# Optimization experiments

Hardware: AMD Instinct MI355X
Metric: run time of the kernel (lower is better)

The kernel has to match this reference:

```python
import jax, jax.numpy as jnp
import numpy as np

EMBED = 192
HEADS = 6
WIN = (7, 7, 7)
B = 256
NW = 64  # number of distinct window masks; b // NW = true batch
N = WIN[0] * WIN[1] * WIN[2]  # 343 tokens per window


def _rel_pos_index(win):
    # Faithful port of the torch buffer construction.
    coords = np.stack(np.meshgrid(np.arange(win[0]), np.arange(win[1]), np.arange(win[2]), indexing='ij'))
    cf = coords.reshape(3, -1)                     # [3, N]
    rel = cf[:, :, None] - cf[:, None, :]          # [3, N, N]
    rel = rel.transpose(1, 2, 0).copy()            # [N, N, 3]
    rel[..., 0] += win[0] - 1
    rel[..., 1] += win[1] - 1
    rel[..., 2] += win[2] - 1
    rel[..., 0] *= (2 * win[1] - 1) * (2 * win[2] - 1)
    rel[..., 1] *= (2 * win[2] - 1)
    return rel.sum(-1).astype(np.int32)            # [N, N]


def setup_inputs() -> dict:
    key = jax.random.key(0)
    ks = jax.random.split(key, 8)
    table_size = (2 * WIN[0] - 1) * (2 * WIN[1] - 1) * (2 * WIN[2] - 1)  # 2197
    return {
        'x_in': jax.random.normal(ks[0], (B, N, EMBED), dtype=jnp.float32),
        'x_cross': jax.random.normal(ks[1], (B, N, EMBED), dtype=jnp.float32),
        'mask': jnp.zeros((NW, N, N), dtype=jnp.float32),
        'q_w': jax.random.normal(ks[2], (EMBED, EMBED), dtype=jnp.float32) * 0.02,
        'kv_w': jax.random.normal(ks[3], (2 * EMBED, EMBED), dtype=jnp.float32) * 0.02,
        'proj_w': jax.random.normal(ks[4], (EMBED, EMBED), dtype=jnp.float32) * 0.02,
        'proj_b': jnp.zeros((EMBED,), dtype=jnp.float32),
        'bias_table': jax.random.normal(ks[5], (table_size, HEADS), dtype=jnp.float32) * 0.02,
        'rel_idx': jnp.asarray(_rel_pos_index(WIN)),
    }


def reference(x_in, x_cross, mask, q_w, kv_w, proj_w, proj_b, bias_table, rel_idx):
    b, n, c = x_in.shape
    h = HEADS
    hd = c // h
    scale = hd ** -0.5
    # Projections (torch Linear: y = x @ W^T), no qkv bias
    q = (x_in @ q_w.T).reshape(b, n, h, hd).transpose(0, 2, 1, 3) * scale   # [b,h,n,hd]
    kv = (x_cross @ kv_w.T).reshape(b, n, 2, h, hd)
    k = kv[:, :, 0].transpose(0, 2, 1, 3)                                   # [b,h,n,hd]
    v = kv[:, :, 1].transpose(0, 2, 1, 3)                                   # [b,h,n,hd]
    attn = jnp.einsum('bhqd,bhkd->bhqk', q, k)                              # [b,h,n,n]
    # Gathered relative position bias
    bias = bias_table[rel_idx[:n, :n].reshape(-1)].reshape(n, n, h).transpose(2, 0, 1)
    attn = attn + bias[None]
    # Window mask add: [b//nw, nw, h, n, n] + [1, nw, 1, n, n]
    nw = mask.shape[0]
    attn = attn.reshape(b // nw, nw, h, n, n) + mask[None, :, None]
    attn = attn.reshape(b, h, n, n)
    attn = jax.nn.softmax(attn, axis=-1)
    x = jnp.einsum('bhqk,bhkd->bhqd', attn, v).transpose(0, 2, 1, 3).reshape(b, n, c)
    return x @ proj_w.T + proj_b
```

## Files before the change

kernel.cpp:

```cpp
#include <hip/hip_runtime.h>

#define NTOK 343
#define NPAD 352
#define CEMB 192
#define NH   6
#define HD   32
#define NB   256
#define NWIN 64

typedef __attribute__((ext_vector_type(8))) short short8;
typedef __attribute__((ext_vector_type(4))) float f32x4;
typedef __attribute__((ext_vector_type(4))) unsigned int uint4v;
typedef __attribute__((ext_vector_type(2))) unsigned int uint2v;

__device__ __forceinline__ unsigned short f2bf(float f) {
    unsigned int u = __builtin_bit_cast(unsigned int, f);
    u += 0x7fffu + ((u >> 16) & 1u);
    return (unsigned short)(u >> 16);
}
__device__ __forceinline__ float bf2f(unsigned short h) {
    unsigned int u = ((unsigned int)h) << 16;
    return __builtin_bit_cast(float, u);
}
__device__ __forceinline__ short8 pack8(float4 f0, float4 f1) {
    short8 r;
    r[0] = (short)f2bf(f0.x); r[1] = (short)f2bf(f0.y);
    r[2] = (short)f2bf(f0.z); r[3] = (short)f2bf(f0.w);
    r[4] = (short)f2bf(f1.x); r[5] = (short)f2bf(f1.y);
    r[6] = (short)f2bf(f1.z); r[7] = (short)f2bf(f1.w);
    return r;
}
__device__ __forceinline__ unsigned int cvt_pk_bf16(float lo, float hi) {
    unsigned int r;
    asm("v_cvt_pk_bf16_f32 %0, %1, %2" : "=v"(r) : "v"(lo), "v"(hi));
    return r;
}

#define LOG2E 1.4426950408889634f

__global__ void prep_weights(const float* __restrict__ qw, const float* __restrict__ kvw,
                             const float* __restrict__ pw,
                             unsigned short* __restrict__ qwb, unsigned short* __restrict__ kvwb,
                             unsigned short* __restrict__ pwb) {
    const float scale = 0.17677669529663689f * LOG2E;
    int idx = blockIdx.x * 256 + threadIdx.x;
    if (idx < 36864)        qwb[idx] = f2bf(qw[idx] * scale);
    else if (idx < 110592)  kvwb[idx - 36864] = f2bf(kvw[idx - 36864]);
    else if (idx < 147456)  pwb[idx - 110592] = f2bf(pw[idx - 110592]);
}

__global__ void prep_biasN(const float* __restrict__ table, const int* __restrict__ rel,
                           unsigned short* __restrict__ biasN) {
    __shared__ int sidx[32 * 33];
    int bid = blockIdx.x;
    int qt = bid / 11, kt = bid - qt * 11;
    int q0 = qt * 32, k0 = kt * 32;
    for (int e = threadIdx.x; e < 1024; e += 256) {
        int i = e >> 5, j = e & 31;
        int q = q0 + i, k = k0 + j;
        sidx[i * 33 + j] = (q < NTOK && k < NTOK) ? rel[q * NTOK + k] : -1;
    }
    __syncthreads();
    for (int h = 0; h < NH; h++) {
        for (int e = threadIdx.x; e < 1024; e += 256) {
            int qq = e >> 5, kk = e & 31;
            int idx = sidx[qq * 33 + kk];
            float v = (idx >= 0) ? table[idx * NH + h] * LOG2E : 0.f;
            biasN[((size_t)h * NPAD + (q0 + qq)) * NPAD + (k0 + kk)] = f2bf(v);
        }
    }
}

__global__ void prep_maskN(const float* __restrict__ mask, unsigned short* __restrict__ maskN) {
    int idx = blockIdx.x * 256 + threadIdx.x;
    int w = idx / (NPAD * NPAD);
    int rem = idx - w * (NPAD * NPAD);
    int q = rem / NPAD, k = rem - q * NPAD;
    float v = (q < NTOK && k < NTOK) ? mask[((size_t)w * NTOK + q) * NTOK + k] * LOG2E : 0.f;
    maskN[idx] = f2bf(v);
}

__global__ __launch_bounds__(512, 2)
void qkv_kernel(const float* __restrict__ x_in, const float* __restrict__ x_cross,
                const unsigned short* __restrict__ qwb, const unsigned short* __restrict__ kvwb,
                unsigned short* __restrict__ Qb, unsigned short* __restrict__ Kb,
                unsigned short* __restrict__ Vtb) {
    extern __shared__ char smem[];
    unsigned short* Ws = (unsigned short*)smem;
    const int tid = threadIdx.x;
    const int wave = tid >> 6, lane = tid & 63;
    const int quad = lane >> 4, l16 = lane & 15;
    const int b = blockIdx.x / 3, o = blockIdx.x % 3;
    const float* xsrc = (o == 0) ? x_in : x_cross;
    const unsigned short* wsrc = (o == 0) ? qwb : (o == 1 ? kvwb : (kvwb + 192 * CEMB));
    const f32x4 zero4 = {0.f, 0.f, 0.f, 0.f};

    for (int i = tid; i < 4608; i += 512) {
        int r = i / 24, c8 = i - r * 24;
        *(short8*)(Ws + r * 200 + c8 * 8) = *(const short8*)(wsrc + (size_t)r * CEMB + c8 * 8);
    }
    __syncthreads();

    for (int mi = 0; mi < 3; mi++) {
        int mt = wave + (mi << 3);
        if (mt >= 22) continue;
        int row = mt * 16 + l16;
        f32x4 acc[12];
#pragma unroll
        for (int nt = 0; nt < 12; nt++) acc[nt] = zero4;
#pragma unroll
        for (int kc = 0; kc < 6; kc++) {
            short8 a = {};
            if (row < NTOK) {
                const float* xp = xsrc + ((size_t)b * NTOK + row) * CEMB + kc * 32 + (quad << 3);
                float4 f0 = *(const float4*)xp;
                float4 f1 = *(const float4*)(xp + 4);
                a = pack8(f0, f1);
            }
#pragma unroll
            for (int nt = 0; nt < 12; nt++) {
                const short8 bf = *(const short8*)(Ws + (nt * 16 + l16) * 200 + kc * 32 + (quad << 3));
                acc[nt] = __builtin_amdgcn_mfma_f32_16x16x32_bf16(a, bf, acc[nt], 0, 0, 0);
            }
        }
        if (o < 2) {
            unsigned short* dst = (o == 0 ? Qb : Kb) + (size_t)b * NPAD * CEMB;
#pragma unroll
            for (int nt = 0; nt < 12; nt++) {
#pragma unroll
                for (int r = 0; r < 4; r++) {
                    int m = mt * 16 + (quad << 2) + r;
                    dst[(size_t)m * CEMB + nt * 16 + l16] = f2bf(acc[nt][r]);
                }
            }
        } else {
#pragma unroll
            for (int nt = 0; nt < 12; nt++) {
                int h = nt >> 1, d = ((nt & 1) << 4) + l16;
#pragma unroll
                for (int r = 0; r < 4; r++) {
                    int m = mt * 16 + (quad << 2) + r;
                    Vtb[(((size_t)b * NH + h) * 32 + d) * 360 + m] = f2bf(acc[nt][r]);
                }
            }
        }
    }
}

__global__ __launch_bounds__(512, 6)
void attn_kernel(const unsigned short* __restrict__ Qb, const unsigned short* __restrict__ Kb,
                 const unsigned short* __restrict__ Vtb,
                 const unsigned short* __restrict__ biasN, const unsigned short* __restrict__ maskN,
                 unsigned short* __restrict__ attnb) {
    extern __shared__ char smem[];
    unsigned short* Ks = (unsigned short*)smem;
    unsigned short* Vt = (unsigned short*)(smem + 28160);

    const int tid = threadIdx.x;
    const int wave = tid >> 6, lane = tid & 63;
    const int quad = lane >> 4, l16 = lane & 15;
    const int q4 = quad << 2, q8 = quad << 3;
    const int p = blockIdx.x;
    const int L = (p & 7) * 192 + (p >> 3);
    const int w = L / 24, r_ = L - w * 24;
    const int b = (r_ / 6) * 64 + w;
    const int h = r_ - (r_ / 6) * 6;
    const f32x4 zero4 = {0.f, 0.f, 0.f, 0.f};

    for (int i = tid; i < 1408; i += 512) {
        int key = i >> 2, part = i & 3;
        *(short8*)(Ks + key * 40 + part * 8) =
            *(const short8*)(Kb + ((size_t)b * NPAD + key) * CEMB + h * 32 + part * 8);
    }
    const unsigned short* vsrc = Vtb + (size_t)(b * NH + h) * 32 * 360;
    for (int i = tid; i < 1440; i += 512) {
        *(short8*)(Vt + i * 8) = *(const short8*)(vsrc + i * 8);
    }
    short8 qa[3] = {};
#pragma unroll
    for (int i = 0; i < 3; i++) {
        int mt = wave + (i << 3);
        if (mt < 22)
            qa[i] = *(const short8*)(Qb + ((size_t)b * NPAD + mt * 16 + l16) * CEMB + h * 32 + q8);
    }
    __syncthreads();

    const unsigned short* biasNp = biasN + (size_t)h * NPAD * NPAD;
    const unsigned short* maskNp = maskN + (size_t)w * NPAD * NPAD;
#pragma unroll
    for (int i = 0; i < 3; i++) {
        int mt = wave + (i << 3);
        if (mt >= 22) continue;
        const int q = mt * 16 + l16;
        const unsigned short* brow = biasNp + (size_t)q * NPAD;
        const unsigned short* mrow = maskNp + (size_t)q * NPAD;
        float rp = 0.f;
        f32x4 o0 = zero4, o1 = zero4;
        ushort4 bt0c = *(const ushort4*)(brow + q4);
        ushort4 mk0c = *(const ushort4*)(mrow + q4);
        ushort4 bt1c = *(const ushort4*)(brow + 16 + q4);
        ushort4 mk1c = *(const ushort4*)(mrow + 16 + q4);
        for (int ch = 0; ch < 11; ch++) {
            const int kb_ = ch * 32;
            const int kbn = (ch < 10) ? kb_ + 32 : kb_;
            ushort4 bt0n = *(const ushort4*)(brow + kbn + q4);
            ushort4 mk0n = *(const ushort4*)(mrow + kbn + q4);
            ushort4 bt1n = *(const ushort4*)(brow + kbn + 16 + q4);
            ushort4 mk1n = *(const ushort4*)(mrow + kbn + 16 + q4);
            const short8 k0f = *(const short8*)(Ks + (kb_ + l16) * 40 + q8);
            const short8 k1f = *(const short8*)(Ks + (kb_ + 16 + l16) * 40 + q8);
            f32x4 s0 = __builtin_amdgcn_mfma_f32_16x16x32_bf16(k0f, qa[i], zero4, 0, 0, 0);
            f32x4 s1 = __builtin_amdgcn_mfma_f32_16x16x32_bf16(k1f, qa[i], zero4, 0, 0, 0);
            float p00 = __builtin_amdgcn_exp2f(s0[0] + bf2f(bt0c.x) + bf2f(mk0c.x));
            float p01 = __builtin_amdgcn_exp2f(s0[1] + bf2f(bt0c.y) + bf2f(mk0c.y));
            float p02 = __builtin_amdgcn_exp2f(s0[2] + bf2f(bt0c.z) + bf2f(mk0c.z));
            float p03 = __builtin_amdgcn_exp2f(s0[3] + bf2f(bt0c.w) + bf2f(mk0c.w));
            float p10 = __builtin_amdgcn_exp2f(s1[0] + bf2f(bt1c.x) + bf2f(mk1c.x));
            float p11 = __builtin_amdgcn_exp2f(s1[1] + bf2f(bt1c.y) + bf2f(mk1c.y));
            float p12 = __builtin_amdgcn_exp2f(s1[2] + bf2f(bt1c.z) + bf2f(mk1c.z));
            float p13 = __builtin_amdgcn_exp2f(s1[3] + bf2f(bt1c.w) + bf2f(mk1c.w));
            if (ch == 10) {
                if (q4 + 0 >= 7) p10 = 0.f;
                if (q4 + 1 >= 7) p11 = 0.f;
                if (q4 + 2 >= 7) p12 = 0.f;
                if (q4 + 3 >= 7) p13 = 0.f;
            }
            rp += ((p00 + p01) + (p02 + p03)) + ((p10 + p11) + (p12 + p13));
            unsigned int c0 = cvt_pk_bf16(p00, p01);
            unsigned int c1 = cvt_pk_bf16(p02, p03);
            unsigned int c2 = cvt_pk_bf16(p10, p11);
            unsigned int c3 = cvt_pk_bf16(p12, p13);
            uint2v sa = __builtin_amdgcn_permlane32_swap(c0, c2, false, false);
            uint2v sb = __builtin_amdgcn_permlane32_swap(c1, c3, false, false);
            uint2v ta = __builtin_amdgcn_permlane16_swap(sa[0], sa[1], false, false);
            uint2v tb = __builtin_amdgcn_permlane16_swap(sb[0], sb[1], false, false);
            const short8 pa = __builtin_bit_cast(short8, (uint4v){ta[0], tb[0], ta[1], tb[1]});
            const short8 v0 = *(const short8*)(Vt + l16 * 360 + kb_ + q8);
            const short8 v1 = *(const short8*)(Vt + (16 + l16) * 360 + kb_ + q8);
            o0 = __builtin_amdgcn_mfma_f32_16x16x32_bf16(pa, v0, o0, 0, 0, 0);
            o1 = __builtin_amdgcn_mfma_f32_16x16x32_bf16(pa, v1, o1, 0, 0, 0);
            bt0c = bt0n; mk0c = mk0n; bt1c = bt1n; mk1c = mk1n;
        }
        rp += __shfl_xor(rp, 16);
        rp += __shfl_xor(rp, 32);
        float inv = 1.f / rp;
#pragma unroll
        for (int r = 0; r < 4; r++) {
            float invr = __shfl(inv, (lane & 48) | (q4 + r));
            int n = mt * 16 + q4 + r;
            if (n < NTOK) {
                size_t base = ((size_t)b * NTOK + n) * CEMB + h * 32;
                attnb[base + l16] = f2bf(o0[r] * invr);
                attnb[base + 16 + l16] = f2bf(o1[r] * invr);
            }
        }
    }
}

__global__ __launch_bounds__(512, 2)
void proj_kernel(const unsigned short* __restrict__ attnb, const unsigned short* __restrict__ pwb,
                 const float* __restrict__ proj_b, float* __restrict__ out) {
    extern __shared__ char smem[];
    unsigned short* Ws = (unsigned short*)smem;
    const int tid = threadIdx.x;
    const int wave = tid >> 6, lane = tid & 63;
    const int quad = lane >> 4, l16 = lane & 15;
    for (int i = tid; i < 4608; i += 512) {
        int r = i / 24, c8 = i - r * 24;
        *(short8*)(Ws + r * 200 + c8 * 8) = *(const short8*)(pwb + (size_t)r * CEMB + c8 * 8);
    }
    float pb[12];
#pragma unroll
    for (int nt = 0; nt < 12; nt++) pb[nt] = proj_b[nt * 16 + l16];
    __syncthreads();

    const int mt = blockIdx.x * 8 + wave;
    const f32x4 zero4 = {0.f, 0.f, 0.f, 0.f};
    f32x4 acc[12];
#pragma unroll
    for (int nt = 0; nt < 12; nt++) acc[nt] = zero4;
#pragma unroll
    for (int ks = 0; ks < 6; ks++) {
        const short8 a = *(const short8*)(attnb + ((size_t)mt * 16 + l16) * CEMB + ks * 32 + (quad << 3));
#pragma unroll
        for (int nt = 0; nt < 12; nt++) {
            const short8 bfrag = *(const short8*)(Ws + (nt * 16 + l16) * 200 + ks * 32 + (quad << 3));
            acc[nt] = __builtin_amdgcn_mfma_f32_16x16x32_bf16(a, bfrag, acc[nt], 0, 0, 0);
        }
    }
#pragma unroll
    for (int nt = 0; nt < 12; nt++) {
#pragma unroll
        for (int r = 0; r < 4; r++) {
            int m = mt * 16 + (quad << 2) + r;
            out[(size_t)m * CEMB + nt * 16 + l16] = acc[nt][r] + pb[nt];
        }
    }
}

extern "C" void kernel_launch(void* const* d_in, const int* in_sizes, int n_in,
                              void* d_out, int out_size, void* d_ws, size_t ws_size,
                              hipStream_t stream) {
    (void)in_sizes; (void)n_in; (void)out_size; (void)ws_size;
    const float* x_in    = (const float*)d_in[0];
    const float* x_cross = (const float*)d_in[1];
    const float* mask    = (const float*)d_in[2];
    const float* q_w     = (const float*)d_in[3];
    const float* kv_w    = (const float*)d_in[4];
    const float* proj_w  = (const float*)d_in[5];
    const float* proj_b  = (const float*)d_in[6];
    const float* btab    = (const float*)d_in[7];
    const int*   rel     = (const int*)d_in[8];
    float* out = (float*)d_out;
    char* ws = (char*)d_ws;

    unsigned short* qwb   = (unsigned short*)(ws + 0);
    unsigned short* kvwb  = (unsigned short*)(ws + 73728);
    unsigned short* pwb   = (unsigned short*)(ws + 221184);
    unsigned short* biasN = (unsigned short*)(ws + 294912);
    unsigned short* maskN = (unsigned short*)(ws + 1781760);
    unsigned short* attnb = (unsigned short*)(ws + 17641472);
    unsigned short* Qb    = (unsigned short*)(ws + 51359744);
    unsigned short* Kb    = (unsigned short*)(ws + 85962752);
    unsigned short* Vtb   = (unsigned short*)(ws + 120565760);

    prep_weights<<<576, 256, 0, stream>>>(q_w, kv_w, proj_w, qwb, kvwb, pwb);
    prep_biasN<<<121, 256, 0, stream>>>(btab, rel, biasN);
    prep_maskN<<<30976, 256, 0, stream>>>(mask, maskN);
    qkv_kernel<<<NB * 3, 512, 76800, stream>>>(x_in, x_cross, qwb, kvwb, Qb, Kb, Vtb);
    attn_kernel<<<NB * NH, 512, 51200, stream>>>(Qb, Kb, Vtb, biasN, maskN, attnb);
    proj_kernel<<<686, 512, 76800, stream>>>(attnb, pwb, proj_b, out);
}
```

Measured before the change: 411.5 us.

## Store bias and mask in MFMA fragment order and fold into accumulator init

```diff
diff --git a/kernel.cpp b/kernel.cpp
--- a/kernel.cpp
+++ b/kernel.cpp
@@ -7,6 +7,7 @@
 #define HD   32
 #define NB   256
 #define NWIN 64
+#define FPLANE 123904
 
 typedef __attribute__((ext_vector_type(8))) short short8;
 typedef __attribute__((ext_vector_type(4))) float f32x4;
@@ -49,55 +50,62 @@
     else if (idx < 147456)  pwb[idx - 110592] = f2bf(pw[idx - 110592]);
 }
 
-__global__ void prep_biasN(const float* __restrict__ table, const int* __restrict__ rel,
-                           unsigned short* __restrict__ biasN) {
-    __shared__ int sidx[32 * 33];
-    int bid = blockIdx.x;
-    int qt = bid / 11, kt = bid - qt * 11;
-    int q0 = qt * 32, k0 = kt * 32;
-    for (int e = threadIdx.x; e < 1024; e += 256) {
-        int i = e >> 5, j = e & 31;
-        int q = q0 + i, k = k0 + j;
-        sidx[i * 33 + j] = (q < NTOK && k < NTOK) ? rel[q * NTOK + k] : -1;
-    }
-    __syncthreads();
-    for (int h = 0; h < NH; h++) {
-        for (int e = threadIdx.x; e < 1024; e += 256) {
-            int qq = e >> 5, kk = e & 31;
-            int idx = sidx[qq * 33 + kk];
-            float v = (idx >= 0) ? table[idx * NH + h] * LOG2E : 0.f;
-            biasN[((size_t)h * NPAD + (q0 + qq)) * NPAD + (k0 + kk)] = f2bf(v);
-        }
-    }
-}
-
-__global__ void prep_maskN(const float* __restrict__ mask, unsigned short* __restrict__ maskN) {
+__global__ void prep_biasF(const float* __restrict__ table, const int* __restrict__ rel,
+                           unsigned short* __restrict__ biasF) {
     int idx = blockIdx.x * 256 + threadIdx.x;
-    int w = idx / (NPAD * NPAD);
-    int rem = idx - w * (NPAD * NPAD);
-    int q = rem / NPAD, k = rem - q * NPAD;
-    float v = (q < NTOK && k < NTOK) ? mask[((size_t)w * NTOK + q) * NTOK + k] * LOG2E : 0.f;
-    maskN[idx] = f2bf(v);
+    int lane = idx & 63;
+    int rest = idx >> 6;
+    int t = rest & 1; rest >>= 1;
+    int ch = rest % 11; rest /= 11;
+    int mt = rest % 22; int h = rest / 22;
+    int q = mt * 16 + (lane & 15);
+    int k0 = ch * 32 + t * 16 + ((lane >> 4) << 2);
+    ushort4 out;
+#pragma unroll
+    for (int r = 0; r < 4; r++) {
+        int k = k0 + r;
+        float v = (q < NTOK && k < NTOK) ? table[rel[q * NTOK + k] * NH + h] * LOG2E : 0.f;
+        ((unsigned short*)&out)[r] = f2bf(v);
+    }
+    *(ushort4*)(biasF + (size_t)idx * 4) = out;
+}
+
+__global__ void prep_maskF(const float* __restrict__ mask, unsigned short* __restrict__ maskF) {
+    int idx = blockIdx.x * 256 + threadIdx.x;
+    int lane = idx & 63;
+    int rest = idx >> 6;
+    int t = rest & 1; rest >>= 1;
+    int ch = rest % 11; rest /= 11;
+    int mt = rest % 22; int w = rest / 22;
+    int q = mt * 16 + (lane & 15);
+    int k0 = ch * 32 + t * 16 + ((lane >> 4) << 2);
+    ushort4 out;
+#pragma unroll
+    for (int r = 0; r < 4; r++) {
+        int k = k0 + r;
+        float v;
+        if (k >= NTOK) v = -60000.f;
+        else if (q < NTOK) v = mask[((size_t)w * NTOK + q) * NTOK + k] * LOG2E;
+        else v = 0.f;
+        ((unsigned short*)&out)[r] = f2bf(v);
+    }
+    *(ushort4*)(maskF + (size_t)idx * 4) = out;
 }
 
 __global__ __launch_bounds__(512, 2)
-void qkv_kernel(const float* __restrict__ x_in, const float* __restrict__ x_cross,
-                const unsigned short* __restrict__ qwb, const unsigned short* __restrict__ kvwb,
-                unsigned short* __restrict__ Qb, unsigned short* __restrict__ Kb,
-                unsigned short* __restrict__ Vtb) {
+void qkv_q_kernel(const float* __restrict__ x_in, const unsigned short* __restrict__ qwb,
+                  unsigned short* __restrict__ Qb) {
     extern __shared__ char smem[];
     unsigned short* Ws = (unsigned short*)smem;
     const int tid = threadIdx.x;
     const int wave = tid >> 6, lane = tid & 63;
     const int quad = lane >> 4, l16 = lane & 15;
-    const int b = blockIdx.x / 3, o = blockIdx.x % 3;
-    const float* xsrc = (o == 0) ? x_in : x_cross;
-    const unsigned short* wsrc = (o == 0) ? qwb : (o == 1 ? kvwb : (kvwb + 192 * CEMB));
+    const int b = blockIdx.x;
     const f32x4 zero4 = {0.f, 0.f, 0.f, 0.f};
 
     for (int i = tid; i < 4608; i += 512) {
         int r = i / 24, c8 = i - r * 24;
-        *(short8*)(Ws + r * 200 + c8 * 8) = *(const short8*)(wsrc + (size_t)r * CEMB + c8 * 8);
+        *(short8*)(Ws + r * 200 + c8 * 8) = *(const short8*)(qwb + (size_t)r * CEMB + c8 * 8);
     }
     __syncthreads();
 
@@ -112,10 +120,8 @@
         for (int kc = 0; kc < 6; kc++) {
             short8 a = {};
             if (row < NTOK) {
-                const float* xp = xsrc + ((size_t)b * NTOK + row) * CEMB + kc * 32 + (quad << 3);
-                float4 f0 = *(const float4*)xp;
-                float4 f1 = *(const float4*)(xp + 4);
-                a = pack8(f0, f1);
+                const float* xp = x_in + ((size_t)b * NTOK + row) * CEMB + kc * 32 + (quad << 3);
+                a = pack8(*(const float4*)xp, *(const float4*)(xp + 4));
             }
 #pragma unroll
             for (int nt = 0; nt < 12; nt++) {
@@ -123,25 +129,104 @@
                 acc[nt] = __builtin_amdgcn_mfma_f32_16x16x32_bf16(a, bf, acc[nt], 0, 0, 0);
             }
         }
-        if (o < 2) {
-            unsigned short* dst = (o == 0 ? Qb : Kb) + (size_t)b * NPAD * CEMB;
+        unsigned short* dst = Qb + (size_t)b * NPAD * CEMB;
+#pragma unroll
+        for (int nt = 0; nt < 12; nt++) {
+#pragma unroll
+            for (int r = 0; r < 4; r++) {
+                int m = mt * 16 + (quad << 2) + r;
+                dst[(size_t)m * CEMB + nt * 16 + l16] = f2bf(acc[nt][r]);
+            }
+        }
+    }
+}
+
+__global__ __launch_bounds__(512, 2)
+void qkv_kv_kernel(const float* __restrict__ x_cross, const unsigned short* __restrict__ kvwb,
+                   unsigned short* __restrict__ Kb, unsigned short* __restrict__ Vtb) {
+    extern __shared__ char smem[];
+    unsigned short* Ws = (unsigned short*)smem;
+    const int tid = threadIdx.x;
+    const int wave = tid >> 6, lane = tid & 63;
+    const int quad = lane >> 4, l16 = lane & 15;
+    const int b = blockIdx.x;
+    const f32x4 zero4 = {0.f, 0.f, 0.f, 0.f};
+
+    for (int i = tid; i < 4608; i += 512) {
+        int r = i / 24, c8 = i - r * 24;
+        *(short8*)(Ws + r * 200 + c8 * 8) = *(const short8*)(kvwb + (size_t)r * CEMB + c8 * 8);
+    }
+
+    short8 a[3][6];
+#pragma unroll
+    for (int mi = 0; mi < 3; mi++) {
+        int mt = wave + (mi << 3);
+        int row = mt * 16 + l16;
+#pragma unroll
+        for (int kc = 0; kc < 6; kc++) {
+            a[mi][kc] = (short8){};
+            if (mt < 22 && row < NTOK) {
+                const float* xp = x_cross + ((size_t)b * NTOK + row) * CEMB + kc * 32 + (quad << 3);
+                a[mi][kc] = pack8(*(const float4*)xp, *(const float4*)(xp + 4));
+            }
+        }
+    }
+    __syncthreads();
+
+#pragma unroll
+    for (int mi = 0; mi < 3; mi++) {
+        int mt = wave + (mi << 3);
+        if (mt >= 22) continue;
+        f32x4 acc[12];
+#pragma unroll
+        for (int nt = 0; nt < 12; nt++) acc[nt] = zero4;
+#pragma unroll
+        for (int kc = 0; kc < 6; kc++) {
 #pragma unroll
             for (int nt = 0; nt < 12; nt++) {
-#pragma unroll
-                for (int r = 0; r < 4; r++) {
-                    int m = mt * 16 + (quad << 2) + r;
-                    dst[(size_t)m * CEMB + nt * 16 + l16] = f2bf(acc[nt][r]);
-                }
-            }
-        } else {
+                const short8 bf = *(const short8*)(Ws + (nt * 16 + l16) * 200 + kc * 32 + (quad << 3));
+                acc[nt] = __builtin_amdgcn_mfma_f32_16x16x32_bf16(a[mi][kc], bf, acc[nt], 0, 0, 0);
+            }
+        }
+        unsigned short* dst = Kb + (size_t)b * NPAD * CEMB;
+#pragma unroll
+        for (int nt = 0; nt < 12; nt++) {
+#pragma unroll
+            for (int r = 0; r < 4; r++) {
+                int m = mt * 16 + (quad << 2) + r;
+                dst[(size_t)m * CEMB + nt * 16 + l16] = f2bf(acc[nt][r]);
+            }
+        }
+    }
+    __syncthreads();
+    for (int i = tid; i < 4608; i += 512) {
+        int r = i / 24, c8 = i - r * 24;
+        *(short8*)(Ws + r * 200 + c8 * 8) = *(const short8*)(kvwb + (size_t)(192 + r) * CEMB + c8 * 8);
+    }
+    __syncthreads();
+
+#pragma unroll
+    for (int mi = 0; mi < 3; mi++) {
+        int mt = wave + (mi << 3);
+        if (mt >= 22) continue;
+        f32x4 acc[12];
+#pragma unroll
+        for (int nt = 0; nt < 12; nt++) acc[nt] = zero4;
+#pragma unroll
+        for (int kc = 0; kc < 6; kc++) {
 #pragma unroll
             for (int nt = 0; nt < 12; nt++) {
-                int h = nt >> 1, d = ((nt & 1) << 4) + l16;
-#pragma unroll
-                for (int r = 0; r < 4; r++) {
-                    int m = mt * 16 + (quad << 2) + r;
-                    Vtb[(((size_t)b * NH + h) * 32 + d) * 360 + m] = f2bf(acc[nt][r]);
-                }
+                const short8 bf = *(const short8*)(Ws + (nt * 16 + l16) * 200 + kc * 32 + (quad << 3));
+                acc[nt] = __builtin_amdgcn_mfma_f32_16x16x32_bf16(a[mi][kc], bf, acc[nt], 0, 0, 0);
+            }
+        }
+#pragma unroll
+        for (int nt = 0; nt < 12; nt++) {
+            int h = nt >> 1, d = ((nt & 1) << 4) + l16;
+#pragma unroll
+            for (int r = 0; r < 4; r++) {
+                int m = mt * 16 + (quad << 2) + r;
+                Vtb[(((size_t)b * NH + h) * 32 + d) * 360 + m] = f2bf(acc[nt][r]);
             }
         }
     }
@@ -150,7 +235,7 @@
 __global__ __launch_bounds__(512, 6)
 void attn_kernel(const unsigned short* __restrict__ Qb, const unsigned short* __restrict__ Kb,
                  const unsigned short* __restrict__ Vtb,
-                 const unsigned short* __restrict__ biasN, const unsigned short* __restrict__ maskN,
+                 const unsigned short* __restrict__ biasF, const unsigned short* __restrict__ maskF,
                  unsigned short* __restrict__ attnb) {
     extern __shared__ char smem[];
     unsigned short* Ks = (unsigned short*)smem;
@@ -185,53 +270,55 @@
     }
     __syncthreads();
 
-    const unsigned short* biasNp = biasN + (size_t)h * NPAD * NPAD;
-    const unsigned short* maskNp = maskN + (size_t)w * NPAD * NPAD;
+    const unsigned short* bF = biasF + (size_t)h * FPLANE;
+    const unsigned short* mF = maskF + (size_t)w * FPLANE;
+    const int lane4 = lane << 2;
 #pragma unroll
     for (int i = 0; i < 3; i++) {
         int mt = wave + (i << 3);
         if (mt >= 22) continue;
-        const int q = mt * 16 + l16;
-        const unsigned short* brow = biasNp + (size_t)q * NPAD;
-        const unsigned short* mrow = maskNp + (size_t)q * NPAD;
         float rp = 0.f;
         f32x4 o0 = zero4, o1 = zero4;
-        ushort4 bt0c = *(const ushort4*)(brow + q4);
-        ushort4 mk0c = *(const ushort4*)(mrow + q4);
-        ushort4 bt1c = *(const ushort4*)(brow + 16 + q4);
-        ushort4 mk1c = *(const ushort4*)(mrow + 16 + q4);
+        int off = mt * 5632;
+        ushort4 bt0c = *(const ushort4*)(bF + off + lane4);
+        ushort4 mk0c = *(const ushort4*)(mF + off + lane4);
+        ushort4 bt1c = *(const ushort4*)(bF + off + 256 + lane4);
+        ushort4 mk1c = *(const ushort4*)(mF + off + 256 + lane4);
         for (int ch = 0; ch < 11; ch++) {
             const int kb_ = ch * 32;
-            const int kbn = (ch < 10) ? kb_ + 32 : kb_;
-            ushort4 bt0n = *(const ushort4*)(brow + kbn + q4);
-            ushort4 mk0n = *(const ushort4*)(mrow + kbn + q4);
-            ushort4 bt1n = *(const ushort4*)(brow + kbn + 16 + q4);
-            ushort4 mk1n = *(const ushort4*)(mrow + kbn + 16 + q4);
+            const int offn = (ch < 10) ? off + 512 : off;
+            ushort4 bt0n = *(const ushort4*)(bF + offn + lane4);
+            ushort4 mk0n = *(const ushort4*)(mF + offn + lane4);
+            ushort4 bt1n = *(const ushort4*)(bF + offn + 256 + lane4);
+            ushort4 mk1n = *(const ushort4*)(mF + offn + 256 + lane4);
+            f32x4 c0, c1;
+            c0[0] = bf2f(bt0c.x) + bf2f(mk0c.x);
+            c0[1] = bf2f(bt0c.y) + bf2f(mk0c.y);
+            c0[2] = bf2f(bt0c.z) + bf2f(mk0c.z);
+            c0[3] = bf2f(bt0c.w) + bf2f(mk0c.w);
+            c1[0] = bf2f(bt1c.x) + bf2f(mk1c.x);
+            c1[1] = bf2f(bt1c.y) + bf2f(mk1c.y);
+            c1[2] = bf2f(bt1c.z) + bf2f(mk1c.z);
+            c1[3] = bf2f(bt1c.w) + bf2f(mk1c.w);
             const short8 k0f = *(const short8*)(Ks + (kb_ + l16) * 40 + q8);
             const short8 k1f = *(const short8*)(Ks + (kb_ + 16 + l16) * 40 + q8);
-            f32x4 s0 = __builtin_amdgcn_mfma_f32_16x16x32_bf16(k0f, qa[i], zero4, 0, 0, 0);
-            f32x4 s1 = __builtin_amdgcn_mfma_f32_16x16x32_bf16(k1f, qa[i], zero4, 0, 0, 0);
-            float p00 = __builtin_amdgcn_exp2f(s0[0] + bf2f(bt0c.x) + bf2f(mk0c.x));
-            float p01 = __builtin_amdgcn_exp2f(s0[1] + bf2f(bt0c.y) + bf2f(mk0c.y));
-            float p02 = __builtin_amdgcn_exp2f(s0[2] + bf2f(bt0c.z) + bf2f(mk0c.z));
-            float p03 = __builtin_amdgcn_exp2f(s0[3] + bf2f(bt0c.w) + bf2f(mk0c.w));
-            float p10 = __builtin_amdgcn_exp2f(s1[0] + bf2f(bt1c.x) + bf2f(mk1c.x));
-            float p11 = __builtin_amdgcn_exp2f(s1[1] + bf2f(bt1c.y) + bf2f(mk1c.y));
-            float p12 = __builtin_amdgcn_exp2f(s1[2] + bf2f(bt1c.z) + bf2f(mk1c.z));
-            float p13 = __builtin_amdgcn_exp2f(s1[3] + bf2f(bt1c.w) + bf2f(mk1c.w));
-            if (ch == 10) {
-                if (q4 + 0 >= 7) p10 = 0.f;
-                if (q4 + 1 >= 7) p11 = 0.f;
-                if (q4 + 2 >= 7) p12 = 0.f;
-                if (q4 + 3 >= 7) p13 = 0.f;
-            }
+            f32x4 s0 = __builtin_amdgcn_mfma_f32_16x16x32_bf16(k0f, qa[i], c0, 0, 0, 0);
+            f32x4 s1 = __builtin_amdgcn_mfma_f32_16x16x32_bf16(k1f, qa[i], c1, 0, 0, 0);
+            float p00 = __builtin_amdgcn_exp2f(s0[0]);
+            float p01 = __builtin_amdgcn_exp2f(s0[1]);
+            float p02 = __builtin_amdgcn_exp2f(s0[2]);
+            float p03 = __builtin_amdgcn_exp2f(s0[3]);
+            float p10 = __builtin_amdgcn_exp2f(s1[0]);
+            float p11 = __builtin_amdgcn_exp2f(s1[1]);
+            float p12 = __builtin_amdgcn_exp2f(s1[2]);
+            float p13 = __builtin_amdgcn_exp2f(s1[3]);
             rp += ((p00 + p01) + (p02 + p03)) + ((p10 + p11) + (p12 + p13));
-            unsigned int c0 = cvt_pk_bf16(p00, p01);
-            unsigned int c1 = cvt_pk_bf16(p02, p03);
-            unsigned int c2 = cvt_pk_bf16(p10, p11);
-            unsigned int c3 = cvt_pk_bf16(p12, p13);
-            uint2v sa = __builtin_amdgcn_permlane32_swap(c0, c2, false, false);
-            uint2v sb = __builtin_amdgcn_permlane32_swap(c1, c3, false, false);
+            unsigned int e0 = cvt_pk_bf16(p00, p01);
+            unsigned int e1 = cvt_pk_bf16(p02, p03);
+            unsigned int e2 = cvt_pk_bf16(p10, p11);
+            unsigned int e3 = cvt_pk_bf16(p12, p13);
+            uint2v sa = __builtin_amdgcn_permlane32_swap(e0, e2, false, false);
+            uint2v sb = __builtin_amdgcn_permlane32_swap(e1, e3, false, false);
             uint2v ta = __builtin_amdgcn_permlane16_swap(sa[0], sa[1], false, false);
             uint2v tb = __builtin_amdgcn_permlane16_swap(sb[0], sb[1], false, false);
             const short8 pa = __builtin_bit_cast(short8, (uint4v){ta[0], tb[0], ta[1], tb[1]});
@@ -240,6 +327,7 @@
             o0 = __builtin_amdgcn_mfma_f32_16x16x32_bf16(pa, v0, o0, 0, 0, 0);
             o1 = __builtin_amdgcn_mfma_f32_16x16x32_bf16(pa, v1, o1, 0, 0, 0);
             bt0c = bt0n; mk0c = mk0n; bt1c = bt1n; mk1c = mk1n;
+            off = offn;
         }
         rp += __shfl_xor(rp, 16);
         rp += __shfl_xor(rp, 32);
@@ -317,17 +405,18 @@
     unsigned short* qwb   = (unsigned short*)(ws + 0);
     unsigned short* kvwb  = (unsigned short*)(ws + 73728);
     unsigned short* pwb   = (unsigned short*)(ws + 221184);
-    unsigned short* biasN = (unsigned short*)(ws + 294912);
-    unsigned short* maskN = (unsigned short*)(ws + 1781760);
+    unsigned short* biasF = (unsigned short*)(ws + 294912);
+    unsigned short* maskF = (unsigned short*)(ws + 1781760);
     unsigned short* attnb = (unsigned short*)(ws + 17641472);
     unsigned short* Qb    = (unsigned short*)(ws + 51359744);
     unsigned short* Kb    = (unsigned short*)(ws + 85962752);
     unsigned short* Vtb   = (unsigned short*)(ws + 120565760);
 
     prep_weights<<<576, 256, 0, stream>>>(q_w, kv_w, proj_w, qwb, kvwb, pwb);
-    prep_biasN<<<121, 256, 0, stream>>>(btab, rel, biasN);
-    prep_maskN<<<30976, 256, 0, stream>>>(mask, maskN);
-    qkv_kernel<<<NB * 3, 512, 76800, stream>>>(x_in, x_cross, qwb, kvwb, Qb, Kb, Vtb);
-    attn_kernel<<<NB * NH, 512, 51200, stream>>>(Qb, Kb, Vtb, biasN, maskN, attnb);
+    prep_biasF<<<728, 256, 0, stream>>>(btab, rel, biasF);
+    prep_maskF<<<7744, 256, 0, stream>>>(mask, maskF);
+    qkv_q_kernel<<<NB, 512, 76800, stream>>>(x_in, qwb, Qb);
+    qkv_kv_kernel<<<NB, 512, 76800, stream>>>(x_cross, kvwb, Kb, Vtb);
+    attn_kernel<<<NB * NH, 512, 51200, stream>>>(Qb, Kb, Vtb, biasF, maskF, attnb);
     proj_kernel<<<686, 512, 76800, stream>>>(attnb, pwb, proj_b, out);
 }
```

Measured after the change: 367.0 us. -10.8%, faster.
